# Performance work log

Measured on AMD Instinct MI355X. Metric: run time of the kernel, lower is better.

Reference implementation:

```python
import jax, jax.numpy as jnp
import numpy as np

N = 50000      # nodes
E = 600000     # edges (avg degree 12)
F_IN = 128     # num_features
H = 128        # hidden_feats (== F_IN so both conv layers share weight shapes)
C = 10         # num_classes
L = 2          # num_layers


def setup_inputs() -> dict:
    key = jax.random.key(0)
    ks = jax.random.split(key, 12)
    s = 0.05
    x = jax.random.normal(ks[0], (N, F_IN), dtype=jnp.float32)
    edge_index = jax.random.randint(ks[1], (2, E), 0, N, dtype=jnp.int64)
    # Stacked per-layer TransformerConv params (heads=1): query/key/value/skip linears.
    Wq = jax.random.normal(ks[2], (L, H, F_IN), dtype=jnp.float32) * s
    bq = jax.random.normal(ks[3], (L, H), dtype=jnp.float32) * s
    Wk = jax.random.normal(ks[4], (L, H, F_IN), dtype=jnp.float32) * s
    bk = jax.random.normal(ks[5], (L, H), dtype=jnp.float32) * s
    Wv = jax.random.normal(ks[6], (L, H, F_IN), dtype=jnp.float32) * s
    bv = jax.random.normal(ks[7], (L, H), dtype=jnp.float32) * s
    Ws = jax.random.normal(ks[8], (L, H, F_IN), dtype=jnp.float32) * s
    bs = jax.random.normal(ks[9], (L, H), dtype=jnp.float32) * s
    fc_W = jax.random.normal(ks[10], (C, H), dtype=jnp.float32) * s
    fc_b = jax.random.normal(ks[11], (C,), dtype=jnp.float32) * s
    return {"x": x, "edge_index": edge_index, "Wq": Wq, "bq": bq, "Wk": Wk,
            "bk": bk, "Wv": Wv, "bv": bv, "Ws": Ws, "bs": bs,
            "fc_W": fc_W, "fc_b": fc_b}


def _transformer_conv(h, src, dst, Wq, bq, Wk, bk, Wv, bv, Ws, bs):
    # PyG TransformerConv, heads=1, concat=True, root_weight=True, eval mode.
    d = Wq.shape[0]
    scale = 1.0 / np.sqrt(d).astype(np.float32)
    q = h @ Wq.T + bq          # [N, d]
    k = h @ Wk.T + bk          # [N, d]
    v = h @ Wv.T + bv          # [N, d]
    # per-edge attention score: <q_dst, k_src> / sqrt(d)
    scores = jnp.sum(q[dst] * k[src], axis=-1) * scale   # [E]
    # scatter-softmax over incoming edges of each destination node
    m = jax.ops.segment_max(scores, dst, num_segments=N)           # [N]
    e = jnp.exp(scores - m[dst])                                   # [E]
    denom = jax.ops.segment_sum(e, dst, num_segments=N)            # [N]
    alpha = e / denom[dst]                                         # [E]
    agg = jax.ops.segment_sum(alpha[:, None] * v[src], dst, num_segments=N)  # [N, d]
    return agg + (h @ Ws.T + bs)  # root/skip connection


def reference(x, edge_index, Wq, bq, Wk, bk, Wv, bv, Ws, bs, fc_W, fc_b):
    src = edge_index[0]
    dst = edge_index[1]
    h = x
    for l in range(L):  # fixed small layer loop
        h = _transformer_conv(h, src, dst, Wq[l], bq[l], Wk[l], bk[l],
                              Wv[l], bv[l], Ws[l], bs[l])
        h = jax.nn.relu(h)  # dropout is identity in eval mode
    logits = h @ fc_W.T + fc_b  # [N, C]
    return jax.nn.log_softmax(logits, axis=1)
```

## Files before the change

kernel.cpp:

```cpp
#include <hip/hip_runtime.h>
#include <math.h>

#define N_NODES 50000
#define N_EDGES 600000
#define DIM 128
#define NCLS 10
#define MTILES 391
#define CHUNKS_PER_TILE 2048
#define NB_SCAN 49

typedef _Float16 h2 __attribute__((ext_vector_type(2)));
typedef _Float16 half8 __attribute__((ext_vector_type(8)));
typedef __attribute__((ext_vector_type(4))) float f32x4;

__device__ inline h2 pkh(float a, float b) {
    auto r = __builtin_amdgcn_cvt_pkrtz(a, b);
    return *(h2*)&r;
}
__device__ inline unsigned h2u(h2 v) { return *(unsigned*)&v; }
__device__ inline h2 u2h(unsigned u) { return *(h2*)&u; }

__device__ inline float dot2acc(h2 a, h2 b, float c) {
#if __has_builtin(__builtin_amdgcn_fdot2)
    return __builtin_amdgcn_fdot2(a, b, c, false);
#else
    return fmaf((float)a.x, (float)b.x, fmaf((float)a.y, (float)b.y, c));
#endif
}

__global__ void deg_kernel(const int* __restrict__ dst, int* __restrict__ deg) {
    int e = blockIdx.x * blockDim.x + threadIdx.x;
    if (e < N_EDGES) atomicAdd(&deg[dst[e]], 1);
}

__global__ __launch_bounds__(1024) void scan1_kernel(
        const int* __restrict__ deg, int* __restrict__ row_start,
        int* __restrict__ partials) {
    __shared__ int buf[1024];
    int b = blockIdx.x, t = threadIdx.x;
    int i = b * 1024 + t;
    buf[t] = (i < N_NODES) ? deg[i] : 0;
    __syncthreads();
    for (int off = 1; off < 1024; off <<= 1) {
        int tv = (t >= off) ? buf[t - off] : 0;
        __syncthreads();
        buf[t] += tv;
        __syncthreads();
    }
    if (i < N_NODES) row_start[i + 1] = buf[t];
    if (t == 1023) partials[b] = buf[1023];
}

__global__ __launch_bounds__(1024) void scan3_kernel(
        const int* __restrict__ partials, int* __restrict__ row_start,
        int* __restrict__ cursor) {
    __shared__ int boff_s;
    int b = blockIdx.x, t = threadIdx.x;
    if (t < 64) {
        int v = (t < b) ? partials[t] : 0;
        #pragma unroll
        for (int off = 32; off >= 1; off >>= 1) v += __shfl_xor(v, off);
        if (t == 0) boff_s = v;
    }
    __syncthreads();
    int boff = boff_s;
    int i = b * 1024 + t;
    if (i < N_NODES) {
        int val = row_start[i + 1] + boff;
        row_start[i + 1] = val;
        if (i + 1 < N_NODES) cursor[i + 1] = val;
    }
    if (i == 0) { row_start[0] = 0; cursor[0] = 0; }
}

__global__ void fill_kernel(const int* __restrict__ src, const int* __restrict__ dst,
                            int* __restrict__ cursor, int* __restrict__ col) {
    int e = blockIdx.x * blockDim.x + threadIdx.x;
    if (e < N_EDGES) {
        int pos = atomicAdd(&cursor[dst[e]], 1);
        col[pos] = src[e];
    }
}

__global__ __launch_bounds__(256) void convertw_kernel(
        const float* __restrict__ Wq, const float* __restrict__ Wk,
        const float* __restrict__ Wv, const float* __restrict__ Ws,
        unsigned short* __restrict__ wfrag) {
    int b = blockIdx.x;
    int l = b >> 2, m = b & 3;
    const float* W = (m == 0 ? Wq : m == 1 ? Wk : m == 2 ? Wv : Ws) + l * DIM * DIM;
    unsigned short* out = wfrag + (size_t)b * (CHUNKS_PER_TILE * 8);
    for (int i = threadIdx.x; i < CHUNKS_PER_TILE; i += 256) {
        int tile = i >> 6, lane = i & 63;
        int row = (tile >> 2) * 16 + (lane & 15);
        int k0 = (tile & 3) * 32 + (lane >> 4) * 8;
        const float4* p = (const float4*)(W + row * DIM + k0);
        float4 a = p[0], bb = p[1];
        uint4 o;
        o.x = h2u(pkh(a.x, a.y));  o.y = h2u(pkh(a.z, a.w));
        o.z = h2u(pkh(bb.x, bb.y)); o.w = h2u(pkh(bb.z, bb.w));
        *(uint4*)(out + (size_t)i * 8) = o;
    }
}

template <bool F32IN>
__global__ __launch_bounds__(512) void linear_kernel(
        const void* __restrict__ hb_,
        const unsigned short* __restrict__ wfrag,
        const float* __restrict__ bq, const float* __restrict__ bk,
        const float* __restrict__ bv, const float* __restrict__ bs,
        unsigned short* __restrict__ Qb, unsigned short* __restrict__ Kb,
        unsigned short* __restrict__ Vb, unsigned short* __restrict__ Sb) {
    __shared__ unsigned short hs[16384];
    __shared__ unsigned short wsm[16384];
    int tid = threadIdx.x;
    int tile = blockIdx.x;
    uint4* lh = (uint4*)hs;
    uint4* lw = (uint4*)wsm;
    #pragma unroll
    for (int j = 0; j < 4; ++j) {
        int i = tid + j * 512;
        int s = i >> 6, lane = i & 63;
        int row = tile * 128 + ((s >> 2) << 4) + (lane & 15);
        int k0 = ((s & 3) << 5) + ((lane >> 4) << 3);
        row = row < N_NODES ? row : N_NODES - 1;
        if (F32IN) {
            const float* hf = (const float*)hb_;
            const float4* p = (const float4*)(hf + (size_t)row * DIM + k0);
            float4 a = p[0], bb = p[1];
            uint4 o;
            o.x = h2u(pkh(a.x, a.y));  o.y = h2u(pkh(a.z, a.w));
            o.z = h2u(pkh(bb.x, bb.y)); o.w = h2u(pkh(bb.z, bb.w));
            lh[i] = o;
        } else {
            const unsigned short* hh = (const unsigned short*)hb_;
            lh[i] = *(const uint4*)(hh + (size_t)row * DIM + k0);
        }
    }
    int wave = tid >> 6, lane = tid & 63;
    int node = tile * 128 + wave * 16 + (lane & 15);
    int cq = (lane >> 4) * 4;

    for (int m = 0; m < 4; ++m) {
        const uint4* gw = (const uint4*)(wfrag + (size_t)m * (CHUNKS_PER_TILE * 8));
        __syncthreads();
        #pragma unroll
        for (int j = 0; j < 4; ++j) lw[tid + j * 512] = gw[tid + j * 512];
        __syncthreads();

        f32x4 acc[8];
        #pragma unroll
        for (int nt = 0; nt < 8; ++nt) acc[nt] = (f32x4){0.f, 0.f, 0.f, 0.f};
        #pragma unroll
        for (int ks = 0; ks < 4; ++ks) {
            half8 hbv = *(const half8*)(lh + (wave * 4 + ks) * 64 + lane);
            #pragma unroll
            for (int nt = 0; nt < 8; ++nt)
                acc[nt] = __builtin_amdgcn_mfma_f32_16x16x32_f16(
                              *(const half8*)(lw + (nt * 4 + ks) * 64 + lane),
                              hbv, acc[nt], 0, 0, 0);
        }

        const float* bias = (m == 0 ? bq : m == 1 ? bk : m == 2 ? bv : bs);
        unsigned short* out = (m == 0 ? Qb : m == 1 ? Kb : m == 2 ? Vb : Sb);
        if (node < N_NODES) {
            #pragma unroll
            for (int nt = 0; nt < 8; ++nt) {
                int colv = nt * 16 + cq;
                float4 bi = *(const float4*)(bias + colv);
                uint2 o;
                o.x = h2u(pkh(acc[nt][0] + bi.x, acc[nt][1] + bi.y));
                o.y = h2u(pkh(acc[nt][2] + bi.z, acc[nt][3] + bi.w));
                *(uint2*)(out + (size_t)node * DIM + colv) = o;
            }
        }
    }
}

__global__ __launch_bounds__(256) void attn_kernel(
        const unsigned short* __restrict__ Qb, const unsigned short* __restrict__ Kb,
        const unsigned short* __restrict__ Vb, const unsigned short* __restrict__ Sb,
        const int* __restrict__ row_start, const int* __restrict__ col,
        unsigned short* __restrict__ hout) {
    int wave = threadIdx.x >> 6;
    int lane = threadIdx.x & 63;
    int g = lane >> 4, gl = lane & 15;
    int n = blockIdx.x * 4 + wave;
    if (n >= N_NODES) return;

    const char* Kc = (const char*)Kb + (gl << 4);
    const char* Vc = (const char*)Vb + (gl << 4);
    const float qs = 0.08838834764831843f * 1.4426950408889634f;
    uint4 qu = *(const uint4*)((const char*)Qb + (((unsigned)n) << 8) + (gl << 4));
    h2 q0 = u2h(qu.x), q1 = u2h(qu.y), q2 = u2h(qu.z), q3 = u2h(qu.w);

    int e0 = row_start[n], e1 = row_start[n + 1];
    int deg = e1 - e0;
    const float NEG = -1.0e30f;
    float m = NEG, den = 0.f;
    h2 a0 = (h2)0, a1 = (h2)0, a2 = (h2)0, a3 = (h2)0;

    if (deg > 0) {
        int last = e1 - 1;
        int e = e0 + g;
        int c0 = e < last ? e : last;
        int s = col[c0];
        unsigned off = ((unsigned)s) << 8;
        uint4 kv = *(const uint4*)(Kc + off);
        uint4 vv = *(const uint4*)(Vc + off);
        int en = e + 4;
        int c1 = en < last ? en : last;
        int sn = col[c1];
        int T = (deg + 3) >> 2;
        for (int t = 0; t < T; ++t) {
            bool valid = e < e1;
            uint4 kvc = kv, vvc = vv;
            unsigned offn = ((unsigned)sn) << 8;
            kv = *(const uint4*)(Kc + offn);
            vv = *(const uint4*)(Vc + offn);
            e = en; en = e + 4;
            int c2 = en < last ? en : last;
            sn = col[c2];
            float p = dot2acc(u2h(kvc.x), q0, 0.f);
            p = dot2acc(u2h(kvc.y), q1, p);
            p = dot2acc(u2h(kvc.z), q2, p);
            p = dot2acc(u2h(kvc.w), q3, p);
            p += __shfl_xor(p, 1);
            p += __shfl_xor(p, 2);
            p += __shfl_xor(p, 4);
            p += __shfl_xor(p, 8);
            p = valid ? p * qs : NEG;
            float nm = fmaxf(m, p);
            float fac = exp2f(m - nm);
            float w = valid ? exp2f(p - nm) : 0.f;
            den = fmaf(den, fac, w);
            h2 fw = pkh(fac, w);
            h2 fac2 = { fw.x, fw.x };
            h2 w2 = { fw.y, fw.y };
            a0 = a0 * fac2 + w2 * u2h(vvc.x);
            a1 = a1 * fac2 + w2 * u2h(vvc.y);
            a2 = a2 * fac2 + w2 * u2h(vvc.z);
            a3 = a3 * fac2 + w2 * u2h(vvc.w);
            m = nm;
        }
    }

    float acc[8];
    acc[0] = (float)a0.x; acc[1] = (float)a0.y;
    acc[2] = (float)a1.x; acc[3] = (float)a1.y;
    acc[4] = (float)a2.x; acc[5] = (float)a2.y;
    acc[6] = (float)a3.x; acc[7] = (float)a3.y;
    float M = m;
    M = fmaxf(M, __shfl_xor(M, 16));
    M = fmaxf(M, __shfl_xor(M, 32));
    float fac = exp2f(m - M);
    float d = den * fac;
    d += __shfl_xor(d, 16);
    d += __shfl_xor(d, 32);
    #pragma unroll
    for (int j = 0; j < 8; ++j) {
        float a = acc[j] * fac;
        a += __shfl_xor(a, 16);
        a += __shfl_xor(a, 32);
        acc[j] = a;
    }
    float inv = (d > 0.f) ? 1.f / d : 0.f;

    uint4 su = *(const uint4*)((const char*)Sb + (((unsigned)n) << 8) + (gl << 4));
    if (g == 0) {
        h2 s0 = u2h(su.x), s1 = u2h(su.y), s2 = u2h(su.z), s3 = u2h(su.w);
        uint4 o;
        o.x = h2u(pkh(fmaxf(fmaf(acc[0], inv, (float)s0.x), 0.f),
                      fmaxf(fmaf(acc[1], inv, (float)s0.y), 0.f)));
        o.y = h2u(pkh(fmaxf(fmaf(acc[2], inv, (float)s1.x), 0.f),
                      fmaxf(fmaf(acc[3], inv, (float)s1.y), 0.f)));
        o.z = h2u(pkh(fmaxf(fmaf(acc[4], inv, (float)s2.x), 0.f),
                      fmaxf(fmaf(acc[5], inv, (float)s2.y), 0.f)));
        o.w = h2u(pkh(fmaxf(fmaf(acc[6], inv, (float)s3.x), 0.f),
                      fmaxf(fmaf(acc[7], inv, (float)s3.y), 0.f)));
        *(uint4*)((char*)hout + (((unsigned)n) << 8) + (gl << 4)) = o;
    }
}

__global__ __launch_bounds__(256) void logits_kernel(
        const unsigned short* __restrict__ hb, const float* __restrict__ fcW,
        const float* __restrict__ fcb, float* __restrict__ out) {
    int wave = threadIdx.x >> 6, lane = threadIdx.x & 63;
    int n = blockIdx.x * 4 + wave;
    if (n >= N_NODES) return;
    unsigned hu = ((const unsigned*)hb)[(size_t)n * 64 + lane];
    h2 hh = u2h(hu);
    float hx = (float)hh.x, hy = (float)hh.y;
    float logit[NCLS];
    #pragma unroll
    for (int c = 0; c < NCLS; ++c) {
        float2 w = ((const float2*)(fcW + c * DIM))[lane];
        float p = hx * w.x + hy * w.y;
        #pragma unroll
        for (int off = 32; off >= 1; off >>= 1) p += __shfl_xor(p, off);
        logit[c] = p + fcb[c];
    }
    float mx = logit[0];
    #pragma unroll
    for (int c = 1; c < NCLS; ++c) mx = fmaxf(mx, logit[c]);
    float se = 0.f;
    #pragma unroll
    for (int c = 0; c < NCLS; ++c) se += __expf(logit[c] - mx);
    float lse = mx + logf(se);
    if (lane < NCLS) {
        float myv = 0.f;
        #pragma unroll
        for (int c = 0; c < NCLS; ++c) if (lane == c) myv = logit[c];
        out[(size_t)n * NCLS + lane] = myv - lse;
    }
}

extern "C" void kernel_launch(void* const* d_in, const int* in_sizes, int n_in,
                              void* d_out, int out_size, void* d_ws, size_t ws_size,
                              hipStream_t stream) {
    const float* x   = (const float*)d_in[0];
    const int*   ei  = (const int*)d_in[1];
    const float* Wq  = (const float*)d_in[2];
    const float* bq  = (const float*)d_in[3];
    const float* Wk  = (const float*)d_in[4];
    const float* bk  = (const float*)d_in[5];
    const float* Wv  = (const float*)d_in[6];
    const float* bv  = (const float*)d_in[7];
    const float* Ws  = (const float*)d_in[8];
    const float* bs  = (const float*)d_in[9];
    const float* fcW = (const float*)d_in[10];
    const float* fcb = (const float*)d_in[11];
    const int* src = ei;
    const int* dst = ei + N_EDGES;

    size_t NF = (size_t)N_NODES * DIM;
    unsigned short* Qb = (unsigned short*)d_ws;
    unsigned short* Kb = Qb + NF;
    unsigned short* Vb = Kb + NF;
    unsigned short* Sb = Vb + NF;
    unsigned short* h1 = Sb + NF;
    unsigned short* wfrag = h1 + NF;
    int* ints      = (int*)(wfrag + 8 * CHUNKS_PER_TILE * 8);
    int* row_start = ints;
    int* cursor    = row_start + N_NODES + 1;
    int* col       = cursor + N_NODES;
    int* partials  = col + N_EDGES;

    (void)hipMemsetAsync(cursor, 0, N_NODES * sizeof(int), stream);
    deg_kernel<<<(N_EDGES + 255) / 256, 256, 0, stream>>>(dst, cursor);
    scan1_kernel<<<NB_SCAN, 1024, 0, stream>>>(cursor, row_start, partials);
    scan3_kernel<<<NB_SCAN, 1024, 0, stream>>>(partials, row_start, cursor);
    fill_kernel<<<(N_EDGES + 255) / 256, 256, 0, stream>>>(src, dst, cursor, col);

    convertw_kernel<<<8, 256, 0, stream>>>(Wq, Wk, Wv, Ws, wfrag);

    const int AGRID = (N_NODES + 3) / 4;

    linear_kernel<true><<<MTILES, 512, 0, stream>>>(x, wfrag, bq, bk, bv, bs,
                                                    Qb, Kb, Vb, Sb);
    attn_kernel<<<AGRID, 256, 0, stream>>>(Qb, Kb, Vb, Sb, row_start, col, h1);
    linear_kernel<false><<<MTILES, 512, 0, stream>>>(h1, wfrag + 4 * CHUNKS_PER_TILE * 8,
                                                     bq + DIM, bk + DIM, bv + DIM, bs + DIM,
                                                     Qb, Kb, Vb, Sb);
    attn_kernel<<<AGRID, 256, 0, stream>>>(Qb, Kb, Vb, Sb, row_start, col, h1);
    logits_kernel<<<AGRID, 256, 0, stream>>>(h1, fcW, fcb, (float*)d_out);
}
```

Measured before the change: 269.7 us.

## Interleave K and V rows and batch three edges per attention step with double buffering

The linear kernel now writes K and V into one interleaved buffer with a 256-element row stride, so one source node's key and value sit in the same 512-byte row. The attention kernel processes three edges per group per step with a single online-softmax rescale, and double-buffers two batches of gathers so more memory requests are in flight. The goal is better gather locality and more latency hiding on the random neighbour loads. The cost is higher register pressure, and for low-degree nodes more padded work, since each pair of iterations covers 24 edges per group-of-four lanes.

```diff
diff --git a/kernel.cpp b/kernel.cpp
--- a/kernel.cpp
+++ b/kernel.cpp
@@ -19,6 +19,7 @@
 }
 __device__ inline unsigned h2u(h2 v) { return *(unsigned*)&v; }
 __device__ inline h2 u2h(unsigned u) { return *(h2*)&u; }
+__device__ inline int imin(int a, int b) { return a < b ? a : b; }
 
 __device__ inline float dot2acc(h2 a, h2 b, float c) {
 #if __has_builtin(__builtin_amdgcn_fdot2)
@@ -109,8 +110,8 @@
         const unsigned short* __restrict__ wfrag,
         const float* __restrict__ bq, const float* __restrict__ bk,
         const float* __restrict__ bv, const float* __restrict__ bs,
-        unsigned short* __restrict__ Qb, unsigned short* __restrict__ Kb,
-        unsigned short* __restrict__ Vb, unsigned short* __restrict__ Sb) {
+        unsigned short* __restrict__ Qb, unsigned short* __restrict__ KVb,
+        unsigned short* __restrict__ Sb) {
     __shared__ unsigned short hs[16384];
     __shared__ unsigned short wsm[16384];
     int tid = threadIdx.x;
@@ -141,6 +142,7 @@
     int node = tile * 128 + wave * 16 + (lane & 15);
     int cq = (lane >> 4) * 4;
 
+    #pragma unroll
     for (int m = 0; m < 4; ++m) {
         const uint4* gw = (const uint4*)(wfrag + (size_t)m * (CHUNKS_PER_TILE * 8));
         __syncthreads();
@@ -162,7 +164,12 @@
         }
 
         const float* bias = (m == 0 ? bq : m == 1 ? bk : m == 2 ? bv : bs);
-        unsigned short* out = (m == 0 ? Qb : m == 1 ? Kb : m == 2 ? Vb : Sb);
+        unsigned short* ob;
+        unsigned ostr;
+        if (m == 0)      { ob = Qb;        ostr = DIM; }
+        else if (m == 1) { ob = KVb;       ostr = 256; }
+        else if (m == 2) { ob = KVb + 128; ostr = 256; }
+        else             { ob = Sb;        ostr = DIM; }
         if (node < N_NODES) {
             #pragma unroll
             for (int nt = 0; nt < 8; ++nt) {
@@ -171,15 +178,15 @@
                 uint2 o;
                 o.x = h2u(pkh(acc[nt][0] + bi.x, acc[nt][1] + bi.y));
                 o.y = h2u(pkh(acc[nt][2] + bi.z, acc[nt][3] + bi.w));
-                *(uint2*)(out + (size_t)node * DIM + colv) = o;
+                *(uint2*)(ob + (size_t)node * ostr + colv) = o;
             }
         }
     }
 }
 
 __global__ __launch_bounds__(256) void attn_kernel(
-        const unsigned short* __restrict__ Qb, const unsigned short* __restrict__ Kb,
-        const unsigned short* __restrict__ Vb, const unsigned short* __restrict__ Sb,
+        const unsigned short* __restrict__ Qb, const unsigned short* __restrict__ KVb,
+        const unsigned short* __restrict__ Sb,
         const int* __restrict__ row_start, const int* __restrict__ col,
         unsigned short* __restrict__ hout) {
     int wave = threadIdx.x >> 6;
@@ -188,8 +195,7 @@
     int n = blockIdx.x * 4 + wave;
     if (n >= N_NODES) return;
 
-    const char* Kc = (const char*)Kb + (gl << 4);
-    const char* Vc = (const char*)Vb + (gl << 4);
+    const char* KVc = (const char*)KVb + (gl << 4);
     const float qs = 0.08838834764831843f * 1.4426950408889634f;
     uint4 qu = *(const uint4*)((const char*)Qb + (((unsigned)n) << 8) + (gl << 4));
     h2 q0 = u2h(qu.x), q1 = u2h(qu.y), q2 = u2h(qu.z), q3 = u2h(qu.w);
@@ -200,50 +206,84 @@
     float m = NEG, den = 0.f;
     h2 a0 = (h2)0, a1 = (h2)0, a2 = (h2)0, a3 = (h2)0;
 
+#define LOADB(s0_, s1_, s2_, kA, vA, kB, vB, kC, vC)                      \
+    do {                                                                   \
+        unsigned oA = ((unsigned)(s0_)) << 9;                              \
+        unsigned oB = ((unsigned)(s1_)) << 9;                              \
+        unsigned oC = ((unsigned)(s2_)) << 9;                              \
+        kA = *(const uint4*)(KVc + oA); vA = *(const uint4*)(KVc + oA + 256); \
+        kB = *(const uint4*)(KVc + oB); vB = *(const uint4*)(KVc + oB + 256); \
+        kC = *(const uint4*)(KVc + oC); vC = *(const uint4*)(KVc + oC + 256); \
+    } while (0)
+
+#define EDOT(kv) ({                                                        \
+        float p_ = dot2acc(u2h((kv).x), q0, 0.f);                          \
+        p_ = dot2acc(u2h((kv).y), q1, p_);                                 \
+        p_ = dot2acc(u2h((kv).z), q2, p_);                                 \
+        p_ = dot2acc(u2h((kv).w), q3, p_);                                 \
+        p_ += __shfl_xor(p_, 1); p_ += __shfl_xor(p_, 2);                  \
+        p_ += __shfl_xor(p_, 4); p_ += __shfl_xor(p_, 8);                  \
+        p_; })
+
+#define COMPUTEB(ec_, kA, vA, kB, vB, kC, vC)                              \
+    do {                                                                   \
+        float p0 = EDOT(kA), p1 = EDOT(kB), p2 = EDOT(kC);                 \
+        bool va = (ec_) < e1, vb = (ec_) + 4 < e1, vc = (ec_) + 8 < e1;    \
+        p0 = va ? p0 * qs : NEG;                                           \
+        p1 = vb ? p1 * qs : NEG;                                           \
+        p2 = vc ? p2 * qs : NEG;                                           \
+        float nm = fmaxf(fmaxf(m, p0), fmaxf(p1, p2));                     \
+        float fac = exp2f(m - nm);                                         \
+        float w0 = va ? exp2f(p0 - nm) : 0.f;                              \
+        float w1 = vb ? exp2f(p1 - nm) : 0.f;                              \
+        float w2 = vc ? exp2f(p2 - nm) : 0.f;                              \
+        den = den * fac + w0 + w1 + w2;                                    \
+        h2 f2 = pkh(fac, fac), w02 = pkh(w0, w0),                          \
+           w12 = pkh(w1, w1), w22 = pkh(w2, w2);                           \
+        a0 = a0 * f2 + w02 * u2h(vA.x) + w12 * u2h(vB.x) + w22 * u2h(vC.x); \
+        a1 = a1 * f2 + w02 * u2h(vA.y) + w12 * u2h(vB.y) + w22 * u2h(vC.y); \
+        a2 = a2 * f2 + w02 * u2h(vA.z) + w12 * u2h(vB.z) + w22 * u2h(vC.z); \
+        a3 = a3 * f2 + w02 * u2h(vA.w) + w12 * u2h(vB.w) + w22 * u2h(vC.w); \
+        m = nm;                                                            \
+    } while (0)
+
     if (deg > 0) {
         int last = e1 - 1;
-        int e = e0 + g;
-        int c0 = e < last ? e : last;
-        int s = col[c0];
-        unsigned off = ((unsigned)s) << 8;
-        uint4 kv = *(const uint4*)(Kc + off);
-        uint4 vv = *(const uint4*)(Vc + off);
-        int en = e + 4;
-        int c1 = en < last ? en : last;
-        int sn = col[c1];
-        int T = (deg + 3) >> 2;
-        for (int t = 0; t < T; ++t) {
-            bool valid = e < e1;
-            uint4 kvc = kv, vvc = vv;
-            unsigned offn = ((unsigned)sn) << 8;
-            kv = *(const uint4*)(Kc + offn);
-            vv = *(const uint4*)(Vc + offn);
-            e = en; en = e + 4;
-            int c2 = en < last ? en : last;
-            sn = col[c2];
-            float p = dot2acc(u2h(kvc.x), q0, 0.f);
-            p = dot2acc(u2h(kvc.y), q1, p);
-            p = dot2acc(u2h(kvc.z), q2, p);
-            p = dot2acc(u2h(kvc.w), q3, p);
-            p += __shfl_xor(p, 1);
-            p += __shfl_xor(p, 2);
-            p += __shfl_xor(p, 4);
-            p += __shfl_xor(p, 8);
-            p = valid ? p * qs : NEG;
-            float nm = fmaxf(m, p);
-            float fac = exp2f(m - nm);
-            float w = valid ? exp2f(p - nm) : 0.f;
-            den = fmaf(den, fac, w);
-            h2 fw = pkh(fac, w);
-            h2 fac2 = { fw.x, fw.x };
-            h2 w2 = { fw.y, fw.y };
-            a0 = a0 * fac2 + w2 * u2h(vvc.x);
-            a1 = a1 * fac2 + w2 * u2h(vvc.y);
-            a2 = a2 * fac2 + w2 * u2h(vvc.z);
-            a3 = a3 * fac2 + w2 * u2h(vvc.w);
-            m = nm;
+        int ec = e0 + g;
+        int sA0 = col[imin(ec, last)];
+        int sA1 = col[imin(ec + 4, last)];
+        int sA2 = col[imin(ec + 8, last)];
+        uint4 kA0, vA0, kA1, vA1, kA2, vA2;
+        LOADB(sA0, sA1, sA2, kA0, vA0, kA1, vA1, kA2, vA2);
+        int sB0 = col[imin(ec + 12, last)];
+        int sB1 = col[imin(ec + 16, last)];
+        int sB2 = col[imin(ec + 20, last)];
+        uint4 kB0, vB0, kB1, vB1, kB2, vB2;
+        int B = (deg + 11) / 12;
+        for (int b = 0; b < B; b += 2) {
+            LOADB(sB0, sB1, sB2, kB0, vB0, kB1, vB1, kB2, vB2);
+            {
+                int e2 = ec + 24;
+                sA0 = col[imin(e2, last)];
+                sA1 = col[imin(e2 + 4, last)];
+                sA2 = col[imin(e2 + 8, last)];
+            }
+            COMPUTEB(ec, kA0, vA0, kA1, vA1, kA2, vA2);
+            ec += 12;
+            LOADB(sA0, sA1, sA2, kA0, vA0, kA1, vA1, kA2, vA2);
+            {
+                int e2 = ec + 24;
+                sB0 = col[imin(e2, last)];
+                sB1 = col[imin(e2 + 4, last)];
+                sB2 = col[imin(e2 + 8, last)];
+            }
+            COMPUTEB(ec, kB0, vB0, kB1, vB1, kB2, vB2);
+            ec += 12;
         }
     }
+#undef LOADB
+#undef EDOT
+#undef COMPUTEB
 
     float acc[8];
     acc[0] = (float)a0.x; acc[1] = (float)a0.y;
@@ -334,11 +374,10 @@
     const int* dst = ei + N_EDGES;
 
     size_t NF = (size_t)N_NODES * DIM;
-    unsigned short* Qb = (unsigned short*)d_ws;
-    unsigned short* Kb = Qb + NF;
-    unsigned short* Vb = Kb + NF;
-    unsigned short* Sb = Vb + NF;
-    unsigned short* h1 = Sb + NF;
+    unsigned short* Qb  = (unsigned short*)d_ws;
+    unsigned short* Sb  = Qb + NF;
+    unsigned short* KVb = Sb + NF;
+    unsigned short* h1  = KVb + 2 * NF;
     unsigned short* wfrag = h1 + NF;
     int* ints      = (int*)(wfrag + 8 * CHUNKS_PER_TILE * 8);
     int* row_start = ints;
@@ -357,11 +396,11 @@
     const int AGRID = (N_NODES + 3) / 4;
 
     linear_kernel<true><<<MTILES, 512, 0, stream>>>(x, wfrag, bq, bk, bv, bs,
-                                                    Qb, Kb, Vb, Sb);
-    attn_kernel<<<AGRID, 256, 0, stream>>>(Qb, Kb, Vb, Sb, row_start, col, h1);
+                                                    Qb, KVb, Sb);
+    attn_kernel<<<AGRID, 256, 0, stream>>>(Qb, KVb, Sb, row_start, col, h1);
     linear_kernel<false><<<MTILES, 512, 0, stream>>>(h1, wfrag + 4 * CHUNKS_PER_TILE * 8,
                                                      bq + DIM, bk + DIM, bv + DIM, bs + DIM,
-                                                     Qb, Kb, Vb, Sb);
-    attn_kernel<<<AGRID, 256, 0, stream>>>(Qb, Kb, Vb, Sb, row_start, col, h1);
+                                                     Qb, KVb, Sb);
+    attn_kernel<<<AGRID, 256, 0, stream>>>(Qb, KVb, Sb, row_start, col, h1);
     logits_kernel<<<AGRID, 256, 0, stream>>>(h1, fcW, fcb, (float*)d_out);
 }
```

Result: no change. 268.0 us (-0.6%).
